# Performance work log

Measured on AMD Instinct MI355X. Metric: run time of the kernel, lower is better.

## Reference

```python
import jax, jax.numpy as jnp
import numpy as np

B, T, C, H = 4096, 32, 180, 6
HD = C // H  # 30
EPS = 1e-5

def _ln(x, g, b):
    mu = jnp.mean(x, axis=-1, keepdims=True)
    var = jnp.mean(jnp.square(x - mu), axis=-1, keepdims=True)
    return (x - mu) * jax.lax.rsqrt(var + EPS) * g + b

def setup_inputs() -> dict:
    key = jax.random.key(0)
    ks = jax.random.split(key, 12)
    s_in = 1.0 / np.sqrt(C)
    s_ff = 1.0 / np.sqrt(4 * C)
    return {
        "x": jax.random.normal(ks[0], (B, T, C), jnp.float32),
        "wq": jax.random.normal(ks[1], (H, C, HD), jnp.float32) * s_in,
        "wk": jax.random.normal(ks[2], (H, C, HD), jnp.float32) * s_in,
        "wv": jax.random.normal(ks[3], (H, C, HD), jnp.float32) * s_in,
        "g1": jnp.ones((C,), jnp.float32),
        "be1": jnp.zeros((C,), jnp.float32),
        "g2": jnp.ones((C,), jnp.float32),
        "be2": jnp.zeros((C,), jnp.float32),
        "w1": jax.random.normal(ks[4], (C, 4 * C), jnp.float32) * s_in,
        "b1": jnp.zeros((4 * C,), jnp.float32),
        "w2": jax.random.normal(ks[5], (4 * C, C), jnp.float32) * s_ff,
        "b2": jnp.zeros((C,), jnp.float32),
    }

def reference(x, wq, wk, wv, g1, be1, g2, be2, w1, b1, w2, b2):
    Bv, Tv, Cv = x.shape
    h = _ln(x, g1, be1)
    # batched multi-head QKV (replaces per-head Python loop)
    q = jnp.einsum('btc,hcd->bhtd', h, wq)
    k = jnp.einsum('btc,hcd->bhtd', h, wk)
    v = jnp.einsum('btc,hcd->bhtd', h, wv)
    scores = jnp.einsum('bhtd,bhsd->bhts', q, k) * (HD ** -0.5)
    mask = jnp.tril(jnp.ones((Tv, Tv), bool))
    scores = jnp.where(mask, scores, -jnp.inf)
    attn = jax.nn.softmax(scores, axis=-1)  # dropout off (eval)
    out = jnp.einsum('bhts,bhsd->bhtd', attn, v)
    out = jnp.transpose(out, (0, 2, 1, 3)).reshape(Bv, Tv, Cv)  # concat heads
    x = x + out
    h2 = _ln(x, g2, be2)
    mlp = jax.nn.relu(h2 @ w1 + b1) @ w2 + b2  # dropout off (eval)
    return x + mlp
```

## Files before the change

kernel.cpp:

```cpp
#include <hip/hip_runtime.h>

typedef __attribute__((ext_vector_type(8))) short short8;
typedef __attribute__((ext_vector_type(4))) float f32x4;
typedef unsigned short ushort_t;
typedef unsigned int u32;
typedef unsigned long long u64;

#define MFMA16(a,b,c) __builtin_amdgcn_mfma_f32_16x16x32_bf16((a),(b),(c),0,0,0)

__device__ __forceinline__ ushort_t f2bf(float f){
  union { float f; u32 u; } v; v.f = f;
  u32 r = v.u + 0x7fffu + ((v.u >> 16) & 1u);
  return (ushort_t)(r >> 16);
}
__device__ __forceinline__ float bf2f(ushort_t h){
  union { u32 u; float f; } v; v.u = ((u32)h) << 16; return v.f;
}
__device__ __forceinline__ u64 pack4(float a, float b, float c, float d){
  u32 p0 = (u32)f2bf(a) | ((u32)f2bf(b) << 16);
  u32 p1 = (u32)f2bf(c) | ((u32)f2bf(d) << 16);
  return (u64)p0 | ((u64)p1 << 32);
}
__device__ __forceinline__ u32 pack2(float a, float b){
  return (u32)f2bf(a) | ((u32)f2bf(b) << 16);
}

template<int CTRL>
__device__ __forceinline__ float dpp_add(float x){
  union { float f; int i; } a, b;
  a.f = x;
  b.i = __builtin_amdgcn_update_dpp(a.i, a.i, CTRL, 0xF, 0xF, false);
  return x + b.f;
}
__device__ __forceinline__ float red4_add(float x){
  x = dpp_add<0xB1>(x); x = dpp_add<0x4E>(x);
  return x;
}

#define WQKV_ELEMS (576*192)
#define W1T_ELEMS  (768*192)
#define W2T_ELEMS  (192*768)

#define SH 200
#define SS 40
#define SA 184

__global__ void prep_weights(const float* __restrict__ wq, const float* __restrict__ wk,
                             const float* __restrict__ wv, const float* __restrict__ w1,
                             const float* __restrict__ w2, ushort_t* __restrict__ ws){
  __shared__ float lds_f[11700];
  ushort_t* wqkv = ws;
  ushort_t* w1t = ws + WQKV_ELEMS;
  ushort_t* w2t = w1t + W1T_ELEMS;
  int bid = blockIdx.x, tid = threadIdx.x;

  if (bid < 18){
    int h = bid / 3, m = bid % 3;
    const float* src = ((m == 0) ? wq : (m == 1) ? wk : wv) + (size_t)h*180*30;
    for (int l = 0; l < 22; l++){
      int idx = tid + l*256;
      if (idx < 5400) lds_f[idx] = src[idx];
    }
    __syncthreads();
    u32* dst = (u32*)wqkv;
    for (int l = 0; l < 12; l++){
      int j = tid + l*256;
      int d = j / 96, kp = j - d*96;
      int k0 = 2*kp;
      float f0 = (d < 30 && k0   < 180) ? lds_f[k0*30 + d]     : 0.f;
      float f1 = (d < 30 && k0+1 < 180) ? lds_f[(k0+1)*30 + d] : 0.f;
      dst[(size_t)(h*96 + m*32 + d)*96 + kp] = pack2(f0, f1);
    }
  } else if (bid < 30){
    int n0 = (bid - 18) * 64;
    for (int l = 0; l < 45; l++){
      int idx = tid + l*256;
      int c = idx >> 6, nl = idx & 63;
      int n = n0 + nl;
      lds_f[nl*180 + c] = (n < 720) ? w1[(size_t)c*720 + n] : 0.f;
    }
    __syncthreads();
    u32* dst = (u32*)w1t;
    for (int l = 0; l < 24; l++){
      int j = tid + l*256;
      int nl = j / 96, cp = j - nl*96;
      int c0 = 2*cp;
      float f0 = (c0   < 180) ? lds_f[nl*180 + c0]     : 0.f;
      float f1 = (c0+1 < 180) ? lds_f[nl*180 + c0 + 1] : 0.f;
      dst[(size_t)(n0 + nl)*96 + cp] = pack2(f0, f1);
    }
  } else {
    int c40 = (bid - 30) * 64;
    for (int l = 0; l < 45; l++){
      int idx = tid + l*256;
      int c4l = idx / 180, no = idx - c4l*180;
      lds_f[no*65 + c4l] = (c40 + c4l < 720) ? w2[(size_t)(c40 + c4l)*180 + no] : 0.f;
    }
    __syncthreads();
    u32* dst = (u32*)w2t;
    for (int l = 0; l < 24; l++){
      int j = tid + l*256;
      int no = j >> 5, cp = j & 31;
      float f0 = (no < 180) ? lds_f[no*65 + 2*cp]     : 0.f;
      float f1 = (no < 180) ? lds_f[no*65 + 2*cp + 1] : 0.f;
      dst[(size_t)no*384 + (c40 >> 1) + cp] = pack2(f0, f1);
    }
  }
}

__global__ __launch_bounds__(256, 2)
void block_kernel(const float* __restrict__ x,
                  const float* __restrict__ g1, const float* __restrict__ be1,
                  const float* __restrict__ g2, const float* __restrict__ be2,
                  const float* __restrict__ b1, const float* __restrict__ b2,
                  const ushort_t* __restrict__ wqkv, const ushort_t* __restrict__ w1t,
                  const ushort_t* __restrict__ w2t, float* __restrict__ out){
  __shared__ __align__(16) ushort_t W[64*SH];
  __shared__ __align__(16) ushort_t hn[64*SH];
  __shared__ __align__(16) ushort_t att[64*SA];

  int tid = threadIdx.x;
  int wave = tid >> 6, lane = tid & 63;
  int quad = lane >> 4, c16 = lane & 15;
  long base = (long)blockIdx.x * 11520;

  #pragma unroll 1
  for (int it = 0; it < 12; it++){
    int idx = it*256 + tid;
    if (idx < 2880){
      f32x4 v = *(const f32x4*)(x + base + (long)idx*4);
      int row = (int)(((u32)idx * 745655u) >> 25);
      int col = idx - row*45;
      *(u64*)(hn + row*SH + col*4) = pack4(v.x, v.y, v.z, v.w);
    } else {
      int p = idx - 2880;
      int row = (p*21846) >> 16;
      int g = p - row*3;
      *(u64*)(hn + row*SH + 180 + g*4) = 0ull;
    }
  }
  __syncthreads();

  {
    int row = tid >> 2, sub = tid & 3;
    int c0 = sub*48;
    float s1 = 0.f, s2 = 0.f;
    u64 mv[12];
    #pragma unroll
    for (int gi = 0; gi < 12; gi++){
      mv[gi] = *(const u64*)(hn + row*SH + c0 + gi*4);
      #pragma unroll
      for (int e = 0; e < 4; e++){
        float v = bf2f((ushort_t)(mv[gi] >> (16*e)));
        s1 += v; s2 += v*v;
      }
    }
    s1 = red4_add(s1); s2 = red4_add(s2);
    float mu = s1 * (1.f/180.f);
    float rstd = rsqrtf(s2 * (1.f/180.f) - mu*mu + 1e-5f);
    #pragma unroll
    for (int gi = 0; gi < 12; gi++){
      int c = c0 + gi*4;
      if (c < 180){
        f32x4 gg = *(const f32x4*)(g1 + c);
        f32x4 bb = *(const f32x4*)(be1 + c);
        float v0 = (bf2f((ushort_t)(mv[gi]    )) - mu)*rstd*gg.x + bb.x;
        float v1 = (bf2f((ushort_t)(mv[gi]>>16)) - mu)*rstd*gg.y + bb.y;
        float v2 = (bf2f((ushort_t)(mv[gi]>>32)) - mu)*rstd*gg.z + bb.z;
        float v3 = (bf2f((ushort_t)(mv[gi]>>48)) - mu)*rstd*gg.w + bb.w;
        *(u64*)(hn + row*SH + c) = pack4(v0, v1, v2, v3);
      }
    }
  }
  __syncthreads();

  {
    ushort_t* buf0 = W + wave*(2*32*SS);
    ushort_t* buf1 = buf0 + 32*SS;
    const float scl = 0.18257418583505537f;

    #pragma unroll 1
    for (int jj = 0; jj < 3; jj++){
      int j = wave*3 + jj;
      int bb = (j >= 6) ? 1 : 0;
      int head = j - 6*bb;
      const ushort_t* wbase = wqkv + head*(96*192);

      f32x4 accq[2][2], acck[2][2], accv[2][2];
      #pragma unroll
      for (int i = 0; i < 2; i++)
        #pragma unroll
        for (int jx = 0; jx < 2; jx++){ accq[i][jx]=(f32x4)0.f; acck[i][jx]=(f32x4)0.f; accv[i][jx]=(f32x4)0.f; }

      #pragma unroll 1
      for (int kk = 0; kk < 6; kk++){
        const ushort_t* wk0 = wbase + c16*192 + kk*32 + quad*8;
        short8 aq0 = *(const short8*)(wk0);
        short8 aq1 = *(const short8*)(wk0 + 16*192);
        short8 ak0 = *(const short8*)(wk0 + 32*192);
        short8 ak1 = *(const short8*)(wk0 + 48*192);
        short8 av0 = *(const short8*)(wk0 + 64*192);
        short8 av1 = *(const short8*)(wk0 + 80*192);
        const ushort_t* hb = hn + (bb*32 + c16)*SH + kk*32 + quad*8;
        short8 hf0 = *(const short8*)(hb);
        short8 hf1 = *(const short8*)(hb + 16*SH);
        accq[0][0] = MFMA16(aq0, hf0, accq[0][0]);
        accq[0][1] = MFMA16(aq0, hf1, accq[0][1]);
        accq[1][0] = MFMA16(aq1, hf0, accq[1][0]);
        accq[1][1] = MFMA16(aq1, hf1, accq[1][1]);
        acck[0][0] = MFMA16(ak0, hf0, acck[0][0]);
        acck[0][1] = MFMA16(ak0, hf1, acck[0][1]);
        acck[1][0] = MFMA16(ak1, hf0, acck[1][0]);
        acck[1][1] = MFMA16(ak1, hf1, acck[1][1]);
        accv[0][0] = MFMA16(hf0, av0, accv[0][0]);
        accv[0][1] = MFMA16(hf0, av1, accv[0][1]);
        accv[1][0] = MFMA16(hf1, av0, accv[1][0]);
        accv[1][1] = MFMA16(hf1, av1, accv[1][1]);
      }
      #pragma unroll
      for (int mt = 0; mt < 2; mt++)
        #pragma unroll
        for (int nt = 0; nt < 2; nt++){
          *(u64*)(buf0 + (nt*16 + c16)*SS + mt*16 + quad*4) =
            pack4(accq[mt][nt][0], accq[mt][nt][1], accq[mt][nt][2], accq[mt][nt][3]);
          *(u64*)(buf1 + (nt*16 + c16)*SS + mt*16 + quad*4) =
            pack4(acck[mt][nt][0], acck[mt][nt][1], acck[mt][nt][2], acck[mt][nt][3]);
        }
      f32x4 sacc[2][2];
      #pragma unroll
      for (int i = 0; i < 2; i++){ sacc[i][0]=(f32x4)0.f; sacc[i][1]=(f32x4)0.f; }
      short8 akf[2], bqf[2];
      #pragma unroll
      for (int mt = 0; mt < 2; mt++) akf[mt] = *(const short8*)(buf1 + (mt*16 + c16)*SS + quad*8);
      #pragma unroll
      for (int nt = 0; nt < 2; nt++) bqf[nt] = *(const short8*)(buf0 + (nt*16 + c16)*SS + quad*8);
      #pragma unroll
      for (int mt = 0; mt < 2; mt++)
        #pragma unroll
        for (int nt = 0; nt < 2; nt++)
          sacc[mt][nt] = MFMA16(akf[mt], bqf[nt], sacc[mt][nt]);
      #pragma unroll
      for (int nt = 0; nt < 2; nt++){
        int t = nt*16 + c16;
        float v[8];
        #pragma unroll
        for (int r = 0; r < 4; r++){
          int s0 = quad*4 + r, s1v = 16 + quad*4 + r;
          v[r]   = (s0  > t) ? -1e30f : sacc[0][nt][r]*scl;
          v[4+r] = (s1v > t) ? -1e30f : sacc[1][nt][r]*scl;
        }
        float m = v[0];
        #pragma unroll
        for (int i = 1; i < 8; i++) m = fmaxf(m, v[i]);
        m = fmaxf(m, __shfl_xor(m, 16));
        m = fmaxf(m, __shfl_xor(m, 32));
        float e[8], s = 0.f;
        #pragma unroll
        for (int i = 0; i < 8; i++){ e[i] = __expf(v[i] - m); s += e[i]; }
        s += __shfl_xor(s, 16);
        s += __shfl_xor(s, 32);
        float inv = 1.f / s;
        *(u64*)(buf1 + t*SS +      quad*4) = pack4(e[0]*inv, e[1]*inv, e[2]*inv, e[3]*inv);
        *(u64*)(buf1 + t*SS + 16 + quad*4) = pack4(e[4]*inv, e[5]*inv, e[6]*inv, e[7]*inv);
      }
      #pragma unroll
      for (int mt = 0; mt < 2; mt++)
        #pragma unroll
        for (int nt = 0; nt < 2; nt++)
          *(u64*)(buf0 + (nt*16 + c16)*SS + mt*16 + quad*4) =
            pack4(accv[mt][nt][0], accv[mt][nt][1], accv[mt][nt][2], accv[mt][nt][3]);
      f32x4 oacc[2][2];
      #pragma unroll
      for (int i = 0; i < 2; i++){ oacc[i][0]=(f32x4)0.f; oacc[i][1]=(f32x4)0.f; }
      short8 avf[2], bpf[2];
      #pragma unroll
      for (int mt = 0; mt < 2; mt++) avf[mt] = *(const short8*)(buf0 + (mt*16 + c16)*SS + quad*8);
      #pragma unroll
      for (int nt = 0; nt < 2; nt++) bpf[nt] = *(const short8*)(buf1 + (nt*16 + c16)*SS + quad*8);
      #pragma unroll
      for (int mt = 0; mt < 2; mt++)
        #pragma unroll
        for (int nt = 0; nt < 2; nt++)
          oacc[mt][nt] = MFMA16(avf[mt], bpf[nt], oacc[mt][nt]);
      #pragma unroll
      for (int mt = 0; mt < 2; mt++)
        #pragma unroll
        for (int nt = 0; nt < 2; nt++){
          int t = bb*32 + nt*16 + c16;
          int c = head*30 + mt*16 + quad*4;
          ushort_t* p = att + t*SA + c;
          *(u32*)(p) = pack2(oacc[mt][nt][0], oacc[mt][nt][1]);
          if (mt == 0 || quad < 3)
            *(u32*)(p + 2) = pack2(oacc[mt][nt][2], oacc[mt][nt][3]);
        }
    }
  }
  __syncthreads();

  #pragma unroll 1
  for (int it = 0; it < 12; it++){
    int idx = it*256 + tid;
    if (idx < 2880){
      f32x4 v = *(const f32x4*)(x + base + (long)idx*4);
      int row = (int)(((u32)idx * 745655u) >> 25);
      int col4 = (idx - row*45)*4;
      u64 m = *(const u64*)(att + row*SA + col4);
      v.x += bf2f((ushort_t)(m      ));
      v.y += bf2f((ushort_t)(m >> 16));
      v.z += bf2f((ushort_t)(m >> 32));
      v.w += bf2f((ushort_t)(m >> 48));
      *(f32x4*)(out + base + (long)idx*4) = v;
      *(u64*)(hn + row*SH + col4) = pack4(v.x, v.y, v.z, v.w);
    }
  }
  __syncthreads();

  {
    int row = tid >> 2, sub = tid & 3;
    int c0 = sub*48;
    float s1 = 0.f, s2 = 0.f;
    u64 mv[12];
    #pragma unroll
    for (int gi = 0; gi < 12; gi++){
      mv[gi] = *(const u64*)(hn + row*SH + c0 + gi*4);
      #pragma unroll
      for (int e = 0; e < 4; e++){
        float v = bf2f((ushort_t)(mv[gi] >> (16*e)));
        s1 += v; s2 += v*v;
      }
    }
    s1 = red4_add(s1); s2 = red4_add(s2);
    float mu = s1 * (1.f/180.f);
    float rstd = rsqrtf(s2 * (1.f/180.f) - mu*mu + 1e-5f);
    #pragma unroll
    for (int gi = 0; gi < 12; gi++){
      int c = c0 + gi*4;
      if (c < 180){
        f32x4 gg = *(const f32x4*)(g2 + c);
        f32x4 bb = *(const f32x4*)(be2 + c);
        float v0 = (bf2f((ushort_t)(mv[gi]    )) - mu)*rstd*gg.x + bb.x;
        float v1 = (bf2f((ushort_t)(mv[gi]>>16)) - mu)*rstd*gg.y + bb.y;
        float v2 = (bf2f((ushort_t)(mv[gi]>>32)) - mu)*rstd*gg.z + bb.z;
        float v3 = (bf2f((ushort_t)(mv[gi]>>48)) - mu)*rstd*gg.w + bb.w;
        *(u64*)(hn + row*SH + c) = pack4(v0, v1, v2, v3);
      }
    }
  }
  __syncthreads();

  {
    ushort_t* act = W;
    f32x4 outacc[4][3];
    #pragma unroll
    for (int i = 0; i < 4; i++)
      #pragma unroll
      for (int jx = 0; jx < 3; jx++) outacc[i][jx] = (f32x4)0.f;

    #pragma unroll 1
    for (int ch = 0; ch < 4; ch++){
      f32x4 aacc[3][4];
      #pragma unroll
      for (int i = 0; i < 3; i++)
        #pragma unroll
        for (int jx = 0; jx < 4; jx++) aacc[i][jx] = (f32x4)0.f;
      #pragma unroll 1
      for (int kk = 0; kk < 6; kk++){
        const ushort_t* wb = w1t + (size_t)(ch*192 + wave*48 + c16)*192 + kk*32 + quad*8;
        short8 aw0 = *(const short8*)(wb);
        short8 aw1 = *(const short8*)(wb + 16*192);
        short8 aw2 = *(const short8*)(wb + 32*192);
        const ushort_t* hb = hn + c16*SH + kk*32 + quad*8;
        short8 bh0 = *(const short8*)(hb);
        short8 bh1 = *(const short8*)(hb + 16*SH);
        short8 bh2 = *(const short8*)(hb + 32*SH);
        short8 bh3 = *(const short8*)(hb + 48*SH);
        aacc[0][0] = MFMA16(aw0, bh0, aacc[0][0]);
        aacc[0][1] = MFMA16(aw0, bh1, aacc[0][1]);
        aacc[0][2] = MFMA16(aw0, bh2, aacc[0][2]);
        aacc[0][3] = MFMA16(aw0, bh3, aacc[0][3]);
        aacc[1][0] = MFMA16(aw1, bh0, aacc[1][0]);
        aacc[1][1] = MFMA16(aw1, bh1, aacc[1][1]);
        aacc[1][2] = MFMA16(aw1, bh2, aacc[1][2]);
        aacc[1][3] = MFMA16(aw1, bh3, aacc[1][3]);
        aacc[2][0] = MFMA16(aw2, bh0, aacc[2][0]);
        aacc[2][1] = MFMA16(aw2, bh1, aacc[2][1]);
        aacc[2][2] = MFMA16(aw2, bh2, aacc[2][2]);
        aacc[2][3] = MFMA16(aw2, bh3, aacc[2][3]);
      }
      __syncthreads();
      #pragma unroll
      for (int mi = 0; mi < 3; mi++){
        int nrel = (wave*3+mi)*16 + quad*4;
        int nabs = ch*192 + nrel;
        f32x4 bias = (f32x4)0.f;
        if (nabs < 720) bias = *(const f32x4*)(b1 + nabs);
        #pragma unroll
        for (int tt = 0; tt < 4; tt++){
          float v0 = fmaxf(aacc[mi][tt][0] + bias[0], 0.f);
          float v1 = fmaxf(aacc[mi][tt][1] + bias[1], 0.f);
          float v2 = fmaxf(aacc[mi][tt][2] + bias[2], 0.f);
          float v3 = fmaxf(aacc[mi][tt][3] + bias[3], 0.f);
          *(u64*)(act + (tt*16 + c16)*SH + nrel) = pack4(v0, v1, v2, v3);
        }
      }
      __syncthreads();
      #pragma unroll 1
      for (int kk = 0; kk < 6; kk++){
        const ushort_t* wb = w2t + (size_t)(wave*48 + c16)*768 + ch*192 + kk*32 + quad*8;
        short8 bw0 = *(const short8*)(wb);
        short8 bw1 = *(const short8*)(wb + 16*768);
        short8 bw2 = *(const short8*)(wb + 32*768);
        const ushort_t* ab = act + c16*SH + kk*32 + quad*8;
        short8 aa0 = *(const short8*)(ab);
        short8 aa1 = *(const short8*)(ab + 16*SH);
        short8 aa2 = *(const short8*)(ab + 32*SH);
        short8 aa3 = *(const short8*)(ab + 48*SH);
        outacc[0][0] = MFMA16(aa0, bw0, outacc[0][0]);
        outacc[0][1] = MFMA16(aa0, bw1, outacc[0][1]);
        outacc[0][2] = MFMA16(aa0, bw2, outacc[0][2]);
        outacc[1][0] = MFMA16(aa1, bw0, outacc[1][0]);
        outacc[1][1] = MFMA16(aa1, bw1, outacc[1][1]);
        outacc[1][2] = MFMA16(aa1, bw2, outacc[1][2]);
        outacc[2][0] = MFMA16(aa2, bw0, outacc[2][0]);
        outacc[2][1] = MFMA16(aa2, bw1, outacc[2][1]);
        outacc[2][2] = MFMA16(aa2, bw2, outacc[2][2]);
        outacc[3][0] = MFMA16(aa3, bw0, outacc[3][0]);
        outacc[3][1] = MFMA16(aa3, bw1, outacc[3][1]);
        outacc[3][2] = MFMA16(aa3, bw2, outacc[3][2]);
      }
    }
    #pragma unroll
    for (int ntl = 0; ntl < 3; ntl++){
      int no = wave*48 + ntl*16 + c16;
      if (no < 180){
        float bias = b2[no];
        #pragma unroll
        for (int tt = 0; tt < 4; tt++){
          #pragma unroll
          for (int r = 0; r < 4; r++){
            long a = base + (long)(tt*16 + quad*4 + r)*180 + no;
            out[a] = out[a] + outacc[tt][ntl][r] + bias;
          }
        }
      }
    }
  }
}

extern "C" void kernel_launch(void* const* d_in, const int* in_sizes, int n_in,
                              void* d_out, int out_size, void* d_ws, size_t ws_size,
                              hipStream_t stream) {
  const float* x   = (const float*)d_in[0];
  const float* wq  = (const float*)d_in[1];
  const float* wk  = (const float*)d_in[2];
  const float* wv  = (const float*)d_in[3];
  const float* g1  = (const float*)d_in[4];
  const float* be1 = (const float*)d_in[5];
  const float* g2  = (const float*)d_in[6];
  const float* be2 = (const float*)d_in[7];
  const float* w1  = (const float*)d_in[8];
  const float* b1  = (const float*)d_in[9];
  const float* w2  = (const float*)d_in[10];
  const float* b2  = (const float*)d_in[11];
  ushort_t* ws   = (ushort_t*)d_ws;
  ushort_t* wqkv = ws;
  ushort_t* w1t  = ws + WQKV_ELEMS;
  ushort_t* w2t  = w1t + W1T_ELEMS;
  float* out = (float*)d_out;

  prep_weights<<<42, 256, 0, stream>>>(wq, wk, wv, w1, w2, ws);
  block_kernel<<<2048, 256, 0, stream>>>(x, g1, be1, g2, be2, b1, b2,
                                         wqkv, w1t, w2t, out);
}
```

Measured before the change: 513.8 us.

## Double block to 512 threads and split attention/MLP work across eight waves

```diff
diff --git a/kernel.cpp b/kernel.cpp
--- a/kernel.cpp
+++ b/kernel.cpp
@@ -42,8 +42,7 @@
 #define W2T_ELEMS  (192*768)
 
 #define SH 200
-#define SS 40
-#define SA 184
+#define SS 36
 
 __global__ void prep_weights(const float* __restrict__ wq, const float* __restrict__ wk,
                              const float* __restrict__ wv, const float* __restrict__ w1,
@@ -108,7 +107,7 @@
   }
 }
 
-__global__ __launch_bounds__(256, 2)
+__global__ __launch_bounds__(512, 4)
 void block_kernel(const float* __restrict__ x,
                   const float* __restrict__ g1, const float* __restrict__ be1,
                   const float* __restrict__ g2, const float* __restrict__ be2,
@@ -117,7 +116,7 @@
                   const ushort_t* __restrict__ w2t, float* __restrict__ out){
   __shared__ __align__(16) ushort_t W[64*SH];
   __shared__ __align__(16) ushort_t hn[64*SH];
-  __shared__ __align__(16) ushort_t att[64*SA];
+  __shared__ __align__(16) ushort_t att[64*SH];
 
   int tid = threadIdx.x;
   int wave = tid >> 6, lane = tid & 63;
@@ -125,8 +124,8 @@
   long base = (long)blockIdx.x * 11520;
 
   #pragma unroll 1
-  for (int it = 0; it < 12; it++){
-    int idx = it*256 + tid;
+  for (int it = 0; it < 6; it++){
+    int idx = it*512 + tid;
     if (idx < 2880){
       f32x4 v = *(const f32x4*)(x + base + (long)idx*4);
       int row = (int)(((u32)idx * 745655u) >> 25);
@@ -142,12 +141,12 @@
   __syncthreads();
 
   {
-    int row = tid >> 2, sub = tid & 3;
-    int c0 = sub*48;
+    int row = tid >> 3, sub = tid & 7;
+    int c0 = sub*24;
     float s1 = 0.f, s2 = 0.f;
-    u64 mv[12];
-    #pragma unroll
-    for (int gi = 0; gi < 12; gi++){
+    u64 mv[6];
+    #pragma unroll
+    for (int gi = 0; gi < 6; gi++){
       mv[gi] = *(const u64*)(hn + row*SH + c0 + gi*4);
       #pragma unroll
       for (int e = 0; e < 4; e++){
@@ -155,11 +154,12 @@
         s1 += v; s2 += v*v;
       }
     }
-    s1 = red4_add(s1); s2 = red4_add(s2);
+    s1 = red4_add(s1); s1 += __shfl_xor(s1, 4);
+    s2 = red4_add(s2); s2 += __shfl_xor(s2, 4);
     float mu = s1 * (1.f/180.f);
     float rstd = rsqrtf(s2 * (1.f/180.f) - mu*mu + 1e-5f);
     #pragma unroll
-    for (int gi = 0; gi < 12; gi++){
+    for (int gi = 0; gi < 6; gi++){
       int c = c0 + gi*4;
       if (c < 180){
         f32x4 gg = *(const f32x4*)(g1 + c);
@@ -175,22 +175,22 @@
   __syncthreads();
 
   {
-    ushort_t* buf0 = W + wave*(2*32*SS);
+    int pair = wave >> 1, half = wave & 1;
+    ushort_t* buf0 = W + pair*(2*32*SS);
     ushort_t* buf1 = buf0 + 32*SS;
     const float scl = 0.18257418583505537f;
+    int t = half*16 + c16;
 
     #pragma unroll 1
-    for (int jj = 0; jj < 3; jj++){
-      int j = wave*3 + jj;
+    for (int r3 = 0; r3 < 3; r3++){
+      int j = r3*4 + pair;
       int bb = (j >= 6) ? 1 : 0;
       int head = j - 6*bb;
       const ushort_t* wbase = wqkv + head*(96*192);
 
-      f32x4 accq[2][2], acck[2][2], accv[2][2];
-      #pragma unroll
-      for (int i = 0; i < 2; i++)
-        #pragma unroll
-        for (int jx = 0; jx < 2; jx++){ accq[i][jx]=(f32x4)0.f; acck[i][jx]=(f32x4)0.f; accv[i][jx]=(f32x4)0.f; }
+      f32x4 accq[2], acck[2], accv[2];
+      #pragma unroll
+      for (int i = 0; i < 2; i++){ accq[i]=(f32x4)0.f; acck[i]=(f32x4)0.f; accv[i]=(f32x4)0.f; }
 
       #pragma unroll 1
       for (int kk = 0; kk < 6; kk++){
@@ -201,53 +201,36 @@
         short8 ak1 = *(const short8*)(wk0 + 48*192);
         short8 av0 = *(const short8*)(wk0 + 64*192);
         short8 av1 = *(const short8*)(wk0 + 80*192);
-        const ushort_t* hb = hn + (bb*32 + c16)*SH + kk*32 + quad*8;
-        short8 hf0 = *(const short8*)(hb);
-        short8 hf1 = *(const short8*)(hb + 16*SH);
-        accq[0][0] = MFMA16(aq0, hf0, accq[0][0]);
-        accq[0][1] = MFMA16(aq0, hf1, accq[0][1]);
-        accq[1][0] = MFMA16(aq1, hf0, accq[1][0]);
-        accq[1][1] = MFMA16(aq1, hf1, accq[1][1]);
-        acck[0][0] = MFMA16(ak0, hf0, acck[0][0]);
-        acck[0][1] = MFMA16(ak0, hf1, acck[0][1]);
-        acck[1][0] = MFMA16(ak1, hf0, acck[1][0]);
-        acck[1][1] = MFMA16(ak1, hf1, acck[1][1]);
-        accv[0][0] = MFMA16(hf0, av0, accv[0][0]);
-        accv[0][1] = MFMA16(hf0, av1, accv[0][1]);
-        accv[1][0] = MFMA16(hf1, av0, accv[1][0]);
-        accv[1][1] = MFMA16(hf1, av1, accv[1][1]);
-      }
-      #pragma unroll
-      for (int mt = 0; mt < 2; mt++)
-        #pragma unroll
-        for (int nt = 0; nt < 2; nt++){
-          *(u64*)(buf0 + (nt*16 + c16)*SS + mt*16 + quad*4) =
-            pack4(accq[mt][nt][0], accq[mt][nt][1], accq[mt][nt][2], accq[mt][nt][3]);
-          *(u64*)(buf1 + (nt*16 + c16)*SS + mt*16 + quad*4) =
-            pack4(acck[mt][nt][0], acck[mt][nt][1], acck[mt][nt][2], acck[mt][nt][3]);
-        }
-      f32x4 sacc[2][2];
-      #pragma unroll
-      for (int i = 0; i < 2; i++){ sacc[i][0]=(f32x4)0.f; sacc[i][1]=(f32x4)0.f; }
-      short8 akf[2], bqf[2];
-      #pragma unroll
-      for (int mt = 0; mt < 2; mt++) akf[mt] = *(const short8*)(buf1 + (mt*16 + c16)*SS + quad*8);
-      #pragma unroll
-      for (int nt = 0; nt < 2; nt++) bqf[nt] = *(const short8*)(buf0 + (nt*16 + c16)*SS + quad*8);
-      #pragma unroll
-      for (int mt = 0; mt < 2; mt++)
-        #pragma unroll
-        for (int nt = 0; nt < 2; nt++)
-          sacc[mt][nt] = MFMA16(akf[mt], bqf[nt], sacc[mt][nt]);
-      #pragma unroll
-      for (int nt = 0; nt < 2; nt++){
-        int t = nt*16 + c16;
+        short8 hf = *(const short8*)(hn + (bb*32 + half*16 + c16)*SH + kk*32 + quad*8);
+        accq[0] = MFMA16(aq0, hf, accq[0]);
+        accq[1] = MFMA16(aq1, hf, accq[1]);
+        acck[0] = MFMA16(ak0, hf, acck[0]);
+        acck[1] = MFMA16(ak1, hf, acck[1]);
+        accv[0] = MFMA16(hf, av0, accv[0]);
+        accv[1] = MFMA16(hf, av1, accv[1]);
+      }
+      #pragma unroll
+      for (int mt = 0; mt < 2; mt++){
+        *(u64*)(buf0 + t*SS + mt*16 + quad*4) =
+          pack4(accq[mt][0], accq[mt][1], accq[mt][2], accq[mt][3]);
+        *(u64*)(buf1 + t*SS + mt*16 + quad*4) =
+          pack4(acck[mt][0], acck[mt][1], acck[mt][2], acck[mt][3]);
+      }
+      __syncthreads();
+      f32x4 sacc[2];
+      sacc[0] = (f32x4)0.f; sacc[1] = (f32x4)0.f;
+      short8 akf0 = *(const short8*)(buf1 + c16*SS + quad*8);
+      short8 akf1 = *(const short8*)(buf1 + (16 + c16)*SS + quad*8);
+      short8 bq   = *(const short8*)(buf0 + t*SS + quad*8);
+      sacc[0] = MFMA16(akf0, bq, sacc[0]);
+      sacc[1] = MFMA16(akf1, bq, sacc[1]);
+      {
         float v[8];
         #pragma unroll
         for (int r = 0; r < 4; r++){
           int s0 = quad*4 + r, s1v = 16 + quad*4 + r;
-          v[r]   = (s0  > t) ? -1e30f : sacc[0][nt][r]*scl;
-          v[4+r] = (s1v > t) ? -1e30f : sacc[1][nt][r]*scl;
+          v[r]   = (s0  > t) ? -1e30f : sacc[0][r]*scl;
+          v[4+r] = (s1v > t) ? -1e30f : sacc[1][r]*scl;
         }
         float m = v[0];
         #pragma unroll
@@ -264,47 +247,36 @@
         *(u64*)(buf1 + t*SS + 16 + quad*4) = pack4(e[4]*inv, e[5]*inv, e[6]*inv, e[7]*inv);
       }
       #pragma unroll
-      for (int mt = 0; mt < 2; mt++)
-        #pragma unroll
-        for (int nt = 0; nt < 2; nt++)
-          *(u64*)(buf0 + (nt*16 + c16)*SS + mt*16 + quad*4) =
-            pack4(accv[mt][nt][0], accv[mt][nt][1], accv[mt][nt][2], accv[mt][nt][3]);
-      f32x4 oacc[2][2];
-      #pragma unroll
-      for (int i = 0; i < 2; i++){ oacc[i][0]=(f32x4)0.f; oacc[i][1]=(f32x4)0.f; }
-      short8 avf[2], bpf[2];
-      #pragma unroll
-      for (int mt = 0; mt < 2; mt++) avf[mt] = *(const short8*)(buf0 + (mt*16 + c16)*SS + quad*8);
-      #pragma unroll
-      for (int nt = 0; nt < 2; nt++) bpf[nt] = *(const short8*)(buf1 + (nt*16 + c16)*SS + quad*8);
-      #pragma unroll
-      for (int mt = 0; mt < 2; mt++)
-        #pragma unroll
-        for (int nt = 0; nt < 2; nt++)
-          oacc[mt][nt] = MFMA16(avf[mt], bpf[nt], oacc[mt][nt]);
-      #pragma unroll
-      for (int mt = 0; mt < 2; mt++)
-        #pragma unroll
-        for (int nt = 0; nt < 2; nt++){
-          int t = bb*32 + nt*16 + c16;
-          int c = head*30 + mt*16 + quad*4;
-          ushort_t* p = att + t*SA + c;
-          *(u32*)(p) = pack2(oacc[mt][nt][0], oacc[mt][nt][1]);
-          if (mt == 0 || quad < 3)
-            *(u32*)(p + 2) = pack2(oacc[mt][nt][2], oacc[mt][nt][3]);
-        }
-    }
-  }
-  __syncthreads();
+      for (int nt = 0; nt < 2; nt++)
+        *(u64*)(buf0 + (nt*16 + c16)*SS + half*16 + quad*4) =
+          pack4(accv[nt][0], accv[nt][1], accv[nt][2], accv[nt][3]);
+      __syncthreads();
+      f32x4 oacc[2];
+      oacc[0] = (f32x4)0.f; oacc[1] = (f32x4)0.f;
+      short8 avf0 = *(const short8*)(buf0 + c16*SS + quad*8);
+      short8 avf1 = *(const short8*)(buf0 + (16 + c16)*SS + quad*8);
+      short8 bp   = *(const short8*)(buf1 + t*SS + quad*8);
+      oacc[0] = MFMA16(avf0, bp, oacc[0]);
+      oacc[1] = MFMA16(avf1, bp, oacc[1]);
+      #pragma unroll
+      for (int mt = 0; mt < 2; mt++){
+        ushort_t* p = att + (bb*32 + t)*SH + head*30 + mt*16 + quad*4;
+        *(u32*)(p) = pack2(oacc[mt][0], oacc[mt][1]);
+        if (mt == 0 || quad < 3)
+          *(u32*)(p + 2) = pack2(oacc[mt][2], oacc[mt][3]);
+      }
+      __syncthreads();
+    }
+  }
 
   #pragma unroll 1
-  for (int it = 0; it < 12; it++){
-    int idx = it*256 + tid;
+  for (int it = 0; it < 6; it++){
+    int idx = it*512 + tid;
     if (idx < 2880){
       f32x4 v = *(const f32x4*)(x + base + (long)idx*4);
       int row = (int)(((u32)idx * 745655u) >> 25);
       int col4 = (idx - row*45)*4;
-      u64 m = *(const u64*)(att + row*SA + col4);
+      u64 m = *(const u64*)(att + row*SH + col4);
       v.x += bf2f((ushort_t)(m      ));
       v.y += bf2f((ushort_t)(m >> 16));
       v.z += bf2f((ushort_t)(m >> 32));
@@ -316,12 +288,12 @@
   __syncthreads();
 
   {
-    int row = tid >> 2, sub = tid & 3;
-    int c0 = sub*48;
+    int row = tid >> 3, sub = tid & 7;
+    int c0 = sub*24;
     float s1 = 0.f, s2 = 0.f;
-    u64 mv[12];
-    #pragma unroll
-    for (int gi = 0; gi < 12; gi++){
+    u64 mv[6];
+    #pragma unroll
+    for (int gi = 0; gi < 6; gi++){
       mv[gi] = *(const u64*)(hn + row*SH + c0 + gi*4);
       #pragma unroll
       for (int e = 0; e < 4; e++){
@@ -329,11 +301,12 @@
         s1 += v; s2 += v*v;
       }
     }
-    s1 = red4_add(s1); s2 = red4_add(s2);
+    s1 = red4_add(s1); s1 += __shfl_xor(s1, 4);
+    s2 = red4_add(s2); s2 += __shfl_xor(s2, 4);
     float mu = s1 * (1.f/180.f);
     float rstd = rsqrtf(s2 * (1.f/180.f) - mu*mu + 1e-5f);
     #pragma unroll
-    for (int gi = 0; gi < 12; gi++){
+    for (int gi = 0; gi < 6; gi++){
       int c = c0 + gi*4;
       if (c < 180){
         f32x4 gg = *(const f32x4*)(g2 + c);
@@ -349,96 +322,79 @@
   __syncthreads();
 
   {
-    ushort_t* act = W;
-    f32x4 outacc[4][3];
-    #pragma unroll
-    for (int i = 0; i < 4; i++)
+    int wn  = wave >> 1, wt  = wave & 1;
+    int wt2 = wave >> 2, wno = wave & 3;
+    f32x4 outacc[2][3];
+    #pragma unroll
+    for (int i = 0; i < 2; i++)
       #pragma unroll
       for (int jx = 0; jx < 3; jx++) outacc[i][jx] = (f32x4)0.f;
 
     #pragma unroll 1
     for (int ch = 0; ch < 4; ch++){
-      f32x4 aacc[3][4];
-      #pragma unroll
-      for (int i = 0; i < 3; i++)
-        #pragma unroll
-        for (int jx = 0; jx < 4; jx++) aacc[i][jx] = (f32x4)0.f;
+      ushort_t* actb = (ch & 1) ? att : W;
+      f32x4 aacc[3][2];
+      #pragma unroll
+      for (int i = 0; i < 3; i++){ aacc[i][0]=(f32x4)0.f; aacc[i][1]=(f32x4)0.f; }
       #pragma unroll 1
       for (int kk = 0; kk < 6; kk++){
-        const ushort_t* wb = w1t + (size_t)(ch*192 + wave*48 + c16)*192 + kk*32 + quad*8;
+        const ushort_t* wb = w1t + (size_t)(ch*192 + wn*48 + c16)*192 + kk*32 + quad*8;
         short8 aw0 = *(const short8*)(wb);
         short8 aw1 = *(const short8*)(wb + 16*192);
         short8 aw2 = *(const short8*)(wb + 32*192);
-        const ushort_t* hb = hn + c16*SH + kk*32 + quad*8;
+        const ushort_t* hb = hn + (wt*32 + c16)*SH + kk*32 + quad*8;
         short8 bh0 = *(const short8*)(hb);
         short8 bh1 = *(const short8*)(hb + 16*SH);
-        short8 bh2 = *(const short8*)(hb + 32*SH);
-        short8 bh3 = *(const short8*)(hb + 48*SH);
         aacc[0][0] = MFMA16(aw0, bh0, aacc[0][0]);
         aacc[0][1] = MFMA16(aw0, bh1, aacc[0][1]);
-        aacc[0][2] = MFMA16(aw0, bh2, aacc[0][2]);
-        aacc[0][3] = MFMA16(aw0, bh3, aacc[0][3]);
         aacc[1][0] = MFMA16(aw1, bh0, aacc[1][0]);
         aacc[1][1] = MFMA16(aw1, bh1, aacc[1][1]);
-        aacc[1][2] = MFMA16(aw1, bh2, aacc[1][2]);
-        aacc[1][3] = MFMA16(aw1, bh3, aacc[1][3]);
         aacc[2][0] = MFMA16(aw2, bh0, aacc[2][0]);
         aacc[2][1] = MFMA16(aw2, bh1, aacc[2][1]);
-        aacc[2][2] = MFMA16(aw2, bh2, aacc[2][2]);
-        aacc[2][3] = MFMA16(aw2, bh3, aacc[2][3]);
-      }
-      __syncthreads();
+      }
       #pragma unroll
       for (int mi = 0; mi < 3; mi++){
-        int nrel = (wave*3+mi)*16 + quad*4;
+        int nrel = (wn*3+mi)*16 + quad*4;
         int nabs = ch*192 + nrel;
         f32x4 bias = (f32x4)0.f;
         if (nabs < 720) bias = *(const f32x4*)(b1 + nabs);
         #pragma unroll
-        for (int tt = 0; tt < 4; tt++){
+        for (int tt = 0; tt < 2; tt++){
           float v0 = fmaxf(aacc[mi][tt][0] + bias[0], 0.f);
           float v1 = fmaxf(aacc[mi][tt][1] + bias[1], 0.f);
           float v2 = fmaxf(aacc[mi][tt][2] + bias[2], 0.f);
           float v3 = fmaxf(aacc[mi][tt][3] + bias[3], 0.f);
-          *(u64*)(act + (tt*16 + c16)*SH + nrel) = pack4(v0, v1, v2, v3);
+          *(u64*)(actb + (wt*32 + tt*16 + c16)*SH + nrel) = pack4(v0, v1, v2, v3);
         }
       }
       __syncthreads();
       #pragma unroll 1
       for (int kk = 0; kk < 6; kk++){
-        const ushort_t* wb = w2t + (size_t)(wave*48 + c16)*768 + ch*192 + kk*32 + quad*8;
-        short8 bw0 = *(const short8*)(wb);
-        short8 bw1 = *(const short8*)(wb + 16*768);
-        short8 bw2 = *(const short8*)(wb + 32*768);
-        const ushort_t* ab = act + c16*SH + kk*32 + quad*8;
+        const ushort_t* wb2 = w2t + (size_t)(wno*48 + c16)*768 + ch*192 + kk*32 + quad*8;
+        short8 bw0 = *(const short8*)(wb2);
+        short8 bw1 = *(const short8*)(wb2 + 16*768);
+        short8 bw2 = *(const short8*)(wb2 + 32*768);
+        const ushort_t* ab = actb + (wt2*32 + c16)*SH + kk*32 + quad*8;
         short8 aa0 = *(const short8*)(ab);
         short8 aa1 = *(const short8*)(ab + 16*SH);
-        short8 aa2 = *(const short8*)(ab + 32*SH);
-        short8 aa3 = *(const short8*)(ab + 48*SH);
         outacc[0][0] = MFMA16(aa0, bw0, outacc[0][0]);
         outacc[0][1] = MFMA16(aa0, bw1, outacc[0][1]);
         outacc[0][2] = MFMA16(aa0, bw2, outacc[0][2]);
         outacc[1][0] = MFMA16(aa1, bw0, outacc[1][0]);
         outacc[1][1] = MFMA16(aa1, bw1, outacc[1][1]);
         outacc[1][2] = MFMA16(aa1, bw2, outacc[1][2]);
-        outacc[2][0] = MFMA16(aa2, bw0, outacc[2][0]);
-        outacc[2][1] = MFMA16(aa2, bw1, outacc[2][1]);
-        outacc[2][2] = MFMA16(aa2, bw2, outacc[2][2]);
-        outacc[3][0] = MFMA16(aa3, bw0, outacc[3][0]);
-        outacc[3][1] = MFMA16(aa3, bw1, outacc[3][1]);
-        outacc[3][2] = MFMA16(aa3, bw2, outacc[3][2]);
       }
     }
     #pragma unroll
     for (int ntl = 0; ntl < 3; ntl++){
-      int no = wave*48 + ntl*16 + c16;
+      int no = wno*48 + ntl*16 + c16;
       if (no < 180){
         float bias = b2[no];
         #pragma unroll
-        for (int tt = 0; tt < 4; tt++){
+        for (int tt = 0; tt < 2; tt++){
           #pragma unroll
           for (int r = 0; r < 4; r++){
-            long a = base + (long)(tt*16 + quad*4 + r)*180 + no;
+            long a = base + (long)(wt2*32 + tt*16 + quad*4 + r)*180 + no;
             out[a] = out[a] + outacc[tt][ntl][r] + bias;
           }
         }
@@ -469,6 +425,6 @@
   float* out = (float*)d_out;
 
   prep_weights<<<42, 256, 0, stream>>>(wq, wk, wv, w1, w2, ws);
-  block_kernel<<<2048, 256, 0, stream>>>(x, g1, be1, g2, be2, b1, b2,
+  block_kernel<<<2048, 512, 0, stream>>>(x, g1, be1, g2, be2, b1, b2,
                                          wqkv, w1t, w2t, out);
 }
```

Measured after the change: 684.1 us. +33.2%, slower.

## Stream MLP weight slices into LDS with double-buffered global_load_lds pipeline

Applied to the files above, without the earlier changes.

```diff
diff --git a/kernel.cpp b/kernel.cpp
--- a/kernel.cpp
+++ b/kernel.cpp
@@ -37,6 +37,26 @@
   return x;
 }
 
+__device__ __forceinline__ void gll16(const ushort_t* g, ushort_t* l){
+  __builtin_amdgcn_global_load_lds(
+      (const __attribute__((address_space(1))) void*)g,
+      (__attribute__((address_space(3))) void*)l, 16, 0, 0);
+}
+
+#define WVM(N) do{ \
+  __builtin_amdgcn_sched_barrier(0); \
+  asm volatile("s_waitcnt vmcnt(" #N ")" ::: "memory"); \
+  __builtin_amdgcn_sched_barrier(0); \
+}while(0)
+
+#define STAGE(slice, dbuf) do{ \
+  const ushort_t* _s = (slice) + wave*1536 + (lane << 3); \
+  ushort_t* _d = (dbuf) + wave*1536; \
+  gll16(_s,         _d); \
+  gll16(_s + 512,   _d + 512); \
+  gll16(_s + 1024,  _d + 1024); \
+}while(0)
+
 #define WQKV_ELEMS (576*192)
 #define W1T_ELEMS  (768*192)
 #define W2T_ELEMS  (192*768)
@@ -48,63 +68,41 @@
 __global__ void prep_weights(const float* __restrict__ wq, const float* __restrict__ wk,
                              const float* __restrict__ wv, const float* __restrict__ w1,
                              const float* __restrict__ w2, ushort_t* __restrict__ ws){
-  __shared__ float lds_f[11700];
   ushort_t* wqkv = ws;
-  ushort_t* w1t = ws + WQKV_ELEMS;
-  ushort_t* w2t = w1t + W1T_ELEMS;
-  int bid = blockIdx.x, tid = threadIdx.x;
-
-  if (bid < 18){
-    int h = bid / 3, m = bid % 3;
-    const float* src = ((m == 0) ? wq : (m == 1) ? wk : wv) + (size_t)h*180*30;
-    for (int l = 0; l < 22; l++){
-      int idx = tid + l*256;
-      if (idx < 5400) lds_f[idx] = src[idx];
-    }
-    __syncthreads();
-    u32* dst = (u32*)wqkv;
-    for (int l = 0; l < 12; l++){
-      int j = tid + l*256;
-      int d = j / 96, kp = j - d*96;
-      int k0 = 2*kp;
-      float f0 = (d < 30 && k0   < 180) ? lds_f[k0*30 + d]     : 0.f;
-      float f1 = (d < 30 && k0+1 < 180) ? lds_f[(k0+1)*30 + d] : 0.f;
-      dst[(size_t)(h*96 + m*32 + d)*96 + kp] = pack2(f0, f1);
-    }
-  } else if (bid < 30){
-    int n0 = (bid - 18) * 64;
-    for (int l = 0; l < 45; l++){
-      int idx = tid + l*256;
-      int c = idx >> 6, nl = idx & 63;
-      int n = n0 + nl;
-      lds_f[nl*180 + c] = (n < 720) ? w1[(size_t)c*720 + n] : 0.f;
-    }
-    __syncthreads();
-    u32* dst = (u32*)w1t;
-    for (int l = 0; l < 24; l++){
-      int j = tid + l*256;
-      int nl = j / 96, cp = j - nl*96;
-      int c0 = 2*cp;
-      float f0 = (c0   < 180) ? lds_f[nl*180 + c0]     : 0.f;
-      float f1 = (c0+1 < 180) ? lds_f[nl*180 + c0 + 1] : 0.f;
-      dst[(size_t)(n0 + nl)*96 + cp] = pack2(f0, f1);
-    }
-  } else {
-    int c40 = (bid - 30) * 64;
-    for (int l = 0; l < 45; l++){
-      int idx = tid + l*256;
-      int c4l = idx / 180, no = idx - c4l*180;
-      lds_f[no*65 + c4l] = (c40 + c4l < 720) ? w2[(size_t)(c40 + c4l)*180 + no] : 0.f;
-    }
-    __syncthreads();
-    u32* dst = (u32*)w2t;
-    for (int l = 0; l < 24; l++){
-      int j = tid + l*256;
-      int no = j >> 5, cp = j & 31;
-      float f0 = (no < 180) ? lds_f[no*65 + 2*cp]     : 0.f;
-      float f1 = (no < 180) ? lds_f[no*65 + 2*cp + 1] : 0.f;
-      dst[(size_t)no*384 + (c40 >> 1) + cp] = pack2(f0, f1);
-    }
+  ushort_t* w1s = ws + WQKV_ELEMS;
+  ushort_t* w2s = w1s + W1T_ELEMS;
+  int tid = blockIdx.x * blockDim.x + threadIdx.x;
+  int stride = gridDim.x * blockDim.x;
+  for (int i = tid; i < WQKV_ELEMS; i += stride){
+    int k = i % 192; int row = i / 192;
+    int d = row & 31; int m = (row >> 5) % 3; int h = row / 96;
+    float v = 0.f;
+    if (d < 30 && k < 180){
+      const float* W = (m == 0) ? wq : ((m == 1) ? wk : wv);
+      v = W[(h*180 + k)*30 + d];
+    }
+    wqkv[i] = f2bf(v);
+  }
+  for (int i = tid; i < W1T_ELEMS; i += stride){
+    int slice = i / 6144;  int r = i - slice*6144;
+    int ch = slice / 6, kk = slice - ch*6;
+    int j = r >> 3, e = r & 7;
+    int n = ((j >> 6) << 4) | (j & 15);
+    int cl = (((j >> 4) & 3) << 3) | e;
+    int c = kk*32 + cl;
+    int nab = ch*192 + n;
+    float v = (nab < 720 && c < 180) ? w1[(size_t)c*720 + nab] : 0.f;
+    w1s[i] = f2bf(v);
+  }
+  for (int i = tid; i < W2T_ELEMS; i += stride){
+    int slice = i / 6144;  int r = i - slice*6144;
+    int ch = slice / 6, kk = slice - ch*6;
+    int j = r >> 3, e = r & 7;
+    int n = ((j >> 6) << 4) | (j & 15);
+    int cl = (((j >> 4) & 3) << 3) | e;
+    int c4 = ch*192 + kk*32 + cl;
+    float v = (n < 180 && c4 < 720) ? w2[(size_t)c4*180 + n] : 0.f;
+    w2s[i] = f2bf(v);
   }
 }
 
@@ -113,17 +111,19 @@
                   const float* __restrict__ g1, const float* __restrict__ be1,
                   const float* __restrict__ g2, const float* __restrict__ be2,
                   const float* __restrict__ b1, const float* __restrict__ b2,
-                  const ushort_t* __restrict__ wqkv, const ushort_t* __restrict__ w1t,
-                  const ushort_t* __restrict__ w2t, float* __restrict__ out){
+                  const ushort_t* __restrict__ wqkv, const ushort_t* __restrict__ w1s,
+                  const ushort_t* __restrict__ w2s, float* __restrict__ out){
   __shared__ __align__(16) ushort_t W[64*SH];
   __shared__ __align__(16) ushort_t hn[64*SH];
-  __shared__ __align__(16) ushort_t att[64*SA];
+  __shared__ __align__(16) ushort_t attU[12288];
+  __shared__ __align__(16) float biasL[720];
 
   int tid = threadIdx.x;
   int wave = tid >> 6, lane = tid & 63;
   int quad = lane >> 4, c16 = lane & 15;
   long base = (long)blockIdx.x * 11520;
 
+  if (tid < 180) *(f32x4*)(biasL + (tid << 2)) = *(const f32x4*)(b1 + (tid << 2));
   #pragma unroll 1
   for (int it = 0; it < 12; it++){
     int idx = it*256 + tid;
@@ -288,7 +288,7 @@
         for (int nt = 0; nt < 2; nt++){
           int t = bb*32 + nt*16 + c16;
           int c = head*30 + mt*16 + quad*4;
-          ushort_t* p = att + t*SA + c;
+          ushort_t* p = attU + t*SA + c;
           *(u32*)(p) = pack2(oacc[mt][nt][0], oacc[mt][nt][1]);
           if (mt == 0 || quad < 3)
             *(u32*)(p + 2) = pack2(oacc[mt][nt][2], oacc[mt][nt][3]);
@@ -304,7 +304,7 @@
       f32x4 v = *(const f32x4*)(x + base + (long)idx*4);
       int row = (int)(((u32)idx * 745655u) >> 25);
       int col4 = (idx - row*45)*4;
-      u64 m = *(const u64*)(att + row*SA + col4);
+      u64 m = *(const u64*)(attU + row*SA + col4);
       v.x += bf2f((ushort_t)(m      ));
       v.y += bf2f((ushort_t)(m >> 16));
       v.z += bf2f((ushort_t)(m >> 32));
@@ -329,6 +329,7 @@
         s1 += v; s2 += v*v;
       }
     }
+    STAGE(w1s, attU);
     s1 = red4_add(s1); s2 = red4_add(s2);
     float mu = s1 * (1.f/180.f);
     float rstd = rsqrtf(s2 * (1.f/180.f) - mu*mu + 1e-5f);
@@ -350,6 +351,9 @@
 
   {
     ushort_t* act = W;
+    ushort_t* bufS0 = attU;
+    ushort_t* bufS1 = attU + 6144;
+    int cur = 0;
     f32x4 outacc[4][3];
     #pragma unroll
     for (int i = 0; i < 4; i++)
@@ -363,17 +367,25 @@
       for (int i = 0; i < 3; i++)
         #pragma unroll
         for (int jx = 0; jx < 4; jx++) aacc[i][jx] = (f32x4)0.f;
+
       #pragma unroll 1
       for (int kk = 0; kk < 6; kk++){
-        const ushort_t* wb = w1t + (size_t)(ch*192 + wave*48 + c16)*192 + kk*32 + quad*8;
-        short8 aw0 = *(const short8*)(wb);
-        short8 aw1 = *(const short8*)(wb + 16*192);
-        short8 aw2 = *(const short8*)(wb + 32*192);
+        {
+          const ushort_t* nsrc = (kk < 5) ? (w1s + (ch*6 + kk + 1)*6144)
+                                          : (w2s + (ch*6)*6144);
+          STAGE(nsrc, cur ? bufS0 : bufS1);
+        }
+        WVM(3);
+        const ushort_t* wf = (cur ? bufS1 : bufS0) + wave*1536 + quad*128 + c16*8;
+        short8 aw0 = *(const short8*)(wf);
+        short8 aw1 = *(const short8*)(wf + 512);
+        short8 aw2 = *(const short8*)(wf + 1024);
         const ushort_t* hb = hn + c16*SH + kk*32 + quad*8;
         short8 bh0 = *(const short8*)(hb);
         short8 bh1 = *(const short8*)(hb + 16*SH);
         short8 bh2 = *(const short8*)(hb + 32*SH);
         short8 bh3 = *(const short8*)(hb + 48*SH);
+        __builtin_amdgcn_s_setprio(1);
         aacc[0][0] = MFMA16(aw0, bh0, aacc[0][0]);
         aacc[0][1] = MFMA16(aw0, bh1, aacc[0][1]);
         aacc[0][2] = MFMA16(aw0, bh2, aacc[0][2]);
@@ -386,14 +398,15 @@
         aacc[2][1] = MFMA16(aw2, bh1, aacc[2][1]);
         aacc[2][2] = MFMA16(aw2, bh2, aacc[2][2]);
         aacc[2][3] = MFMA16(aw2, bh3, aacc[2][3]);
-      }
-      __syncthreads();
+        __builtin_amdgcn_s_setprio(0);
+        cur ^= 1;
+      }
       #pragma unroll
       for (int mi = 0; mi < 3; mi++){
         int nrel = (wave*3+mi)*16 + quad*4;
         int nabs = ch*192 + nrel;
         f32x4 bias = (f32x4)0.f;
-        if (nabs < 720) bias = *(const f32x4*)(b1 + nabs);
+        if (nabs < 720) bias = *(const f32x4*)(biasL + nabs);
         #pragma unroll
         for (int tt = 0; tt < 4; tt++){
           float v0 = fmaxf(aacc[mi][tt][0] + bias[0], 0.f);
@@ -406,15 +419,26 @@
       __syncthreads();
       #pragma unroll 1
       for (int kk = 0; kk < 6; kk++){
-        const ushort_t* wb = w2t + (size_t)(wave*48 + c16)*768 + ch*192 + kk*32 + quad*8;
-        short8 bw0 = *(const short8*)(wb);
-        short8 bw1 = *(const short8*)(wb + 16*768);
-        short8 bw2 = *(const short8*)(wb + 32*768);
+        if (ch == 3 && kk == 5){
+          WVM(0);
+        } else {
+          {
+            const ushort_t* nsrc = (kk < 5) ? (w2s + (ch*6 + kk + 1)*6144)
+                                            : (w1s + ((ch+1)*6)*6144);
+            STAGE(nsrc, cur ? bufS0 : bufS1);
+          }
+          WVM(3);
+        }
+        const ushort_t* wf = (cur ? bufS1 : bufS0) + wave*1536 + quad*128 + c16*8;
+        short8 bw0 = *(const short8*)(wf);
+        short8 bw1 = *(const short8*)(wf + 512);
+        short8 bw2 = *(const short8*)(wf + 1024);
         const ushort_t* ab = act + c16*SH + kk*32 + quad*8;
         short8 aa0 = *(const short8*)(ab);
         short8 aa1 = *(const short8*)(ab + 16*SH);
         short8 aa2 = *(const short8*)(ab + 32*SH);
         short8 aa3 = *(const short8*)(ab + 48*SH);
+        __builtin_amdgcn_s_setprio(1);
         outacc[0][0] = MFMA16(aa0, bw0, outacc[0][0]);
         outacc[0][1] = MFMA16(aa0, bw1, outacc[0][1]);
         outacc[0][2] = MFMA16(aa0, bw2, outacc[0][2]);
@@ -427,7 +451,10 @@
         outacc[3][0] = MFMA16(aa3, bw0, outacc[3][0]);
         outacc[3][1] = MFMA16(aa3, bw1, outacc[3][1]);
         outacc[3][2] = MFMA16(aa3, bw2, outacc[3][2]);
-      }
+        __builtin_amdgcn_s_setprio(0);
+        cur ^= 1;
+      }
+      if (ch < 3) __syncthreads();
     }
     #pragma unroll
     for (int ntl = 0; ntl < 3; ntl++){
@@ -464,11 +491,11 @@
   const float* b2  = (const float*)d_in[11];
   ushort_t* ws   = (ushort_t*)d_ws;
   ushort_t* wqkv = ws;
-  ushort_t* w1t  = ws + WQKV_ELEMS;
-  ushort_t* w2t  = w1t + W1T_ELEMS;
+  ushort_t* w1s  = ws + WQKV_ELEMS;
+  ushort_t* w2s  = w1s + W1T_ELEMS;
   float* out = (float*)d_out;
 
-  prep_weights<<<42, 256, 0, stream>>>(wq, wk, wv, w1, w2, ws);
+  prep_weights<<<512, 256, 0, stream>>>(wq, wk, wv, w1, w2, ws);
   block_kernel<<<2048, 256, 0, stream>>>(x, g1, be1, g2, be2, b1, b2,
-                                         wqkv, w1t, w2t, out);
-}
+                                         wqkv, w1s, w2s, out);
+}
```

New measurement: 433.0 us. -15.7%, faster.
